# Kernel tuning notes

Measured on AMD Instinct MI355X. Metric: run time of the kernel, lower is better.

The kernel has to match this reference:

```python
import jax, jax.numpy as jnp
import numpy as np

B, LQ, LK, LS = 2, 2048, 2048, 256
HID, NH = 1024, 16
HD = HID // NH  # head_dim = 64


def setup_inputs() -> dict:
    key = jax.random.key(0)
    ks = jax.random.split(key, 14)
    s = 1.0 / np.sqrt(HID)
    inp = {
        "query": jax.random.normal(ks[0], (B, LQ, HID), jnp.float32),
        "sampled": jax.random.normal(ks[1], (B, LS, HID), jnp.float32),
        "key": jax.random.normal(ks[2], (B, LK, HID), jnp.float32),
        "value": jax.random.normal(ks[3], (B, LK, HID), jnp.float32),
        "Wq": jax.random.uniform(ks[4], (HID, HID), jnp.float32, -s, s),
        "bq": jax.random.uniform(ks[5], (HID,), jnp.float32, -s, s),
        "Wk": jax.random.uniform(ks[6], (HID, HID), jnp.float32, -s, s),
        "bk": jax.random.uniform(ks[7], (HID,), jnp.float32, -s, s),
        "Wv": jax.random.uniform(ks[8], (HID, HID), jnp.float32, -s, s),
        "bv": jax.random.uniform(ks[9], (HID,), jnp.float32, -s, s),
        "Wo": jax.random.uniform(ks[10], (HID, HID), jnp.float32, -s, s),
        "bo": jax.random.uniform(ks[11], (HID,), jnp.float32, -s, s),
        # fresh nn.Linear(LS+LK, LK) created each forward; fan_in = LS+LK
        "rW": jax.random.uniform(ks[12], (LK, LS + LK), jnp.float32, -1.0 / np.sqrt(LS + LK), 1.0 / np.sqrt(LS + LK)),
        "rb": jax.random.uniform(ks[13], (LK,), jnp.float32, -1.0 / np.sqrt(LS + LK), 1.0 / np.sqrt(LS + LK)),
    }
    return inp


def reference(query, sampled, key, value, Wq, bq, Wk, bk, Wv, bv, Wo, bo, rW, rb):
    scale = jnp.sqrt(jnp.float32(HD))
    Q = query @ Wq.T + bq                       # [B, LQ, HID]
    K = key @ Wk.T + bk                         # [B, LK, HID]
    V = value @ Wv.T + bv
    Kc = jnp.concatenate([sampled, K], axis=1)  # [B, LS+LK, HID]
    Vc = jnp.concatenate([sampled, V], axis=1)
    # seq-axis linear: out[b,t,h] = sum_s Kc[b,s,h] * rW[t,s] + rb[t]
    K = jnp.einsum("bsh,ts->bth", Kc, rW) + rb[None, :, None]  # [B, LK, HID]
    V = jnp.einsum("bsh,ts->bth", Vc, rW) + rb[None, :, None]
    # split heads: [B, NH, L, HD]
    Qh = Q.reshape(B, LQ, NH, HD).transpose(0, 2, 1, 3)
    Kh = K.reshape(B, LK, NH, HD).transpose(0, 2, 1, 3)
    Vh = V.reshape(B, LK, NH, HD).transpose(0, 2, 1, 3)
    energy = jnp.einsum("bhqd,bhkd->bhqk", Qh, Kh) / scale
    attention = jax.nn.softmax(energy, axis=-1)  # [B, NH, LQ, LK]
    x = jnp.einsum("bhqk,bhkd->bhqd", attention, Vh)
    x = x.transpose(0, 2, 1, 3).reshape(B, LQ, HID)
    x = x @ Wo.T + bo
    return x, attention
```

## Files before the change

### kernel.cpp

```cpp
#include <hip/hip_runtime.h>
#include <cstdint>
#include <cstddef>

#define NB   2
#define LQ   2048
#define LKK  2048
#define LS   256
#define HID  1024
#define NH   16
#define LSK  2304

#define DEV __device__ __forceinline__

typedef __bf16 bf16x8 __attribute__((ext_vector_type(8)));
typedef __bf16 bf16x4 __attribute__((ext_vector_type(4)));
typedef float  f32x4  __attribute__((ext_vector_type(4)));
typedef unsigned short us8 __attribute__((ext_vector_type(8)));

DEV unsigned short f2bf(float f) {
  unsigned int u = __builtin_bit_cast(unsigned int, f);
  u = (u + 0x7fffu + ((u >> 16) & 1u)) >> 16;
  return (unsigned short)u;
}
DEV bf16x8 ld_frag(const void* p) {
  uint4 v = *(const uint4*)p;
  return __builtin_bit_cast(bf16x8, v);
}
DEV void gload_lds16(const unsigned short* g, unsigned short* l) {
  __builtin_amdgcn_global_load_lds((const __attribute__((address_space(1))) unsigned int*)g,
                                   (__attribute__((address_space(3))) unsigned int*)l,
                                   16, 0, 0);
}
DEV float fexp2(float x) { float r; asm("v_exp_f32 %0, %1" : "=v"(r) : "v"(x)); return r; }

struct CastParams { const float* src[8]; unsigned short* dst[8]; int end8[8]; int total8; };

__global__ __launch_bounds__(256)
void cast_samp(CastParams p, const float* __restrict__ samp,
               unsigned short* __restrict__ KcT, unsigned short* __restrict__ VcT) {
  __shared__ unsigned short tl[64][65];
  const int tid = threadIdx.x;
  if (blockIdx.x < 128) {
    const int bid = blockIdx.x;
    const int st = bid & 3, nt = (bid >> 2) & 15, b = bid >> 6;
    const int nl = tid & 63, sq = tid >> 6;
#pragma unroll
    for (int j = 0; j < 16; ++j) {
      int sl = sq * 16 + j;
      tl[sl][nl] = f2bf(samp[(size_t)(b * LS + st * 64 + sl) * HID + nt * 64 + nl]);
    }
    __syncthreads();
#pragma unroll
    for (int wv = 0; wv < 2; ++wv) {
      int idx = wv * 256 + tid;
      int n_local = idx >> 3, sc = idx & 7;
      us8 v;
#pragma unroll
      for (int j = 0; j < 8; ++j) v[j] = tl[sc * 8 + j][n_local];
      size_t o = (size_t)(b * HID + nt * 64 + n_local) * LSK + st * 64 + sc * 8;
      *(us8*)(KcT + o) = v;
      *(us8*)(VcT + o) = v;
    }
    return;
  }
  const int stride = (gridDim.x - 128) * blockDim.x;
  for (int i = (blockIdx.x - 128) * blockDim.x + tid; i < p.total8; i += stride) {
    int s = 0;
    while (i >= p.end8[s]) ++s;
    int base = s ? p.end8[s - 1] : 0;
    size_t off = (size_t)(i - base) * 8;
    const float4* q = (const float4*)(p.src[s] + off);
    float4 a = q[0], b = q[1];
    us8 o;
    o[0] = f2bf(a.x); o[1] = f2bf(a.y); o[2] = f2bf(a.z); o[3] = f2bf(a.w);
    o[4] = f2bf(b.x); o[5] = f2bf(b.y); o[6] = f2bf(b.z); o[7] = f2bf(b.w);
    *(us8*)(p.dst[s] + off) = o;
  }
}

struct GDesc {
  const unsigned short* A;
  const unsigned short* BT;
  const float* bias;
  void* out0;
  void* out1;
  int ldo, moff, K, flags;
  float oscale;
};
struct GParams { GDesc d[6]; int per_z; int nt_n; int chunk; };

__global__ __launch_bounds__(256, 2)
void gemm_multi(GParams p) {
  __shared__ unsigned short lA[128 * 64];
  __shared__ unsigned short lB[128 * 64];
  const int bid = blockIdx.x;
  const int wid = (bid & 7) * p.chunk + (bid >> 3);
  const int z = wid / p.per_z;
  const int r = wid - z * p.per_z;
  const int n0 = (r % p.nt_n) * 128;
  const int m0 = (r / p.nt_n) * 128;
  const GDesc g = p.d[z];
  const int tid = threadIdx.x, l = tid & 63, w = tid >> 6;
  const int wr = w >> 1, wc = w & 1;
  const int K = g.K;
  const unsigned short* A = g.A;
  const unsigned short* BT = g.BT;
  f32x4 acc[4][4] = {};
  const int nk = K >> 6;
  for (int kt = 0; kt < nk; ++kt) {
    const int k0 = kt << 6;
#pragma unroll
    for (int it = 0; it < 4; ++it) {
      int s = it * 256 + tid;
      int t = s >> 3, c = s & 7, g2 = c ^ (t & 7);
      gload_lds16(A + (size_t)(m0 + t) * K + (k0 + g2 * 8), lA + (size_t)s * 8);
      gload_lds16(BT + (size_t)(n0 + t) * K + (k0 + g2 * 8), lB + (size_t)s * 8);
    }
    __syncthreads();
#pragma unroll
    for (int ks = 0; ks < 2; ++ks) {
      bf16x8 af[4], bfr[4];
#pragma unroll
      for (int mi = 0; mi < 4; ++mi) {
        int row = wr * 64 + mi * 16 + (l & 15);
        int ch = (ks * 4 + (l >> 4)) ^ (row & 7);
        af[mi] = ld_frag((const char*)lA + row * 128 + ch * 16);
      }
#pragma unroll
      for (int ni = 0; ni < 4; ++ni) {
        int row = wc * 64 + ni * 16 + (l & 15);
        int ch = (ks * 4 + (l >> 4)) ^ (row & 7);
        bfr[ni] = ld_frag((const char*)lB + row * 128 + ch * 16);
      }
#pragma unroll
      for (int mi = 0; mi < 4; ++mi)
#pragma unroll
        for (int ni = 0; ni < 4; ++ni)
          acc[mi][ni] = __builtin_amdgcn_mfma_f32_16x16x32_bf16(af[mi], bfr[ni], acc[mi][ni], 0, 0, 0);
    }
    __syncthreads();
  }
  const int epi = g.flags & 15, brow = (g.flags >> 4) & 1;
  const int r4 = (l >> 4) * 4;
#pragma unroll
  for (int mi = 0; mi < 4; ++mi) {
    const int mbase = m0 + wr * 64 + mi * 16 + r4;
#pragma unroll
    for (int ni = 0; ni < 4; ++ni) {
      const int n = n0 + wc * 64 + ni * 16 + (l & 15);
      f32x4 v = acc[mi][ni];
      if (brow) {
#pragma unroll
        for (int rr = 0; rr < 4; ++rr) v[rr] = (v[rr] + g.bias[mbase + rr]) * g.oscale;
      } else {
        const float bn = g.bias[n];
#pragma unroll
        for (int rr = 0; rr < 4; ++rr) v[rr] = (v[rr] + bn) * g.oscale;
      }
      if (epi == 0) {
        unsigned short* o = (unsigned short*)g.out0;
#pragma unroll
        for (int rr = 0; rr < 4; ++rr) o[(size_t)(mbase + rr) * g.ldo + n] = f2bf(v[rr]);
      } else if (epi == 1) {
        unsigned short* o = (unsigned short*)g.out0;
        ushort4 pk;
        pk.x = f2bf(v[0]); pk.y = f2bf(v[1]); pk.z = f2bf(v[2]); pk.w = f2bf(v[3]);
        *(ushort4*)(o + (size_t)n * g.ldo + g.moff + mbase) = pk;
      } else if (epi == 2) {
        float* o = (float*)g.out0;
#pragma unroll
        for (int rr = 0; rr < 4; ++rr) o[(size_t)(mbase + rr) * g.ldo + n] = v[rr];
      } else {
        if (n < 2048) {
          unsigned short* o = (unsigned short*)g.out0 + (size_t)(n >> 10) * LQ * HID;
#pragma unroll
          for (int rr = 0; rr < 4; ++rr) o[(size_t)(mbase + rr) * HID + (n & 1023)] = f2bf(v[rr]);
        } else {
          unsigned short* o = (unsigned short*)g.out1 + (size_t)((n >> 10) - 2) * HID * LKK;
          ushort4 pk;
          pk.x = f2bf(v[0]); pk.y = f2bf(v[1]); pk.z = f2bf(v[2]); pk.w = f2bf(v[3]);
          *(ushort4*)(o + (size_t)(n & 1023) * LKK + mbase) = pk;
        }
      }
    }
  }
}

__global__ __launch_bounds__(256, 2)
void attn_fused(const unsigned short* __restrict__ Qb, const unsigned short* __restrict__ Kn,
                const unsigned short* __restrict__ Vt, float* __restrict__ attn_out,
                unsigned short* __restrict__ xpre) {
  __shared__ unsigned short smem[24576];
  const int tid = threadIdx.x, l = tid & 63, w = tid >> 6;
  const int bid = blockIdx.x;
  const int wid = (bid & 7) * 64 + (bid >> 3);
  const int qt = wid & 15, bh = wid >> 4, b = bh >> 4, h = bh & 15;
  const unsigned short* Qg = Qb + (size_t)(b * LQ + qt * 128) * HID + h * 64;
  const unsigned short* Kg = Kn + (size_t)(b * LKK) * HID + h * 64;
  const unsigned short* Vg = Vt + ((size_t)b * HID + h * 64) * LKK;
  unsigned short* const lK0 = smem;
  unsigned short* const lK1 = smem + 4096;
  unsigned short* const lV0 = smem + 8192;
  unsigned short* const lV1 = smem + 12288;
  unsigned short* const bufA = smem;
  unsigned short* const bufB = smem + 8192;
  unsigned short* const lPw = smem + 16384 + w * 2048;

#pragma unroll
  for (int it = 0; it < 4; ++it) {
    int s = it * 256 + tid, t = s >> 3, c = s & 7, g2 = c ^ (t & 7);
    gload_lds16(Qg + (size_t)t * HID + g2 * 8, smem + (size_t)s * 8);
  }
  __syncthreads();
  bf16x8 qf[2][2];
#pragma unroll
  for (int qi = 0; qi < 2; ++qi)
#pragma unroll
    for (int ds = 0; ds < 2; ++ds) {
      int row = w * 32 + qi * 16 + (l & 15);
      int ch = (ds * 4 + (l >> 4)) ^ (row & 7);
      qf[qi][ds] = ld_frag((const char*)smem + row * 128 + ch * 16);
    }
  __syncthreads();

  auto stageK128 = [&](int kt, unsigned short* dst) {
#pragma unroll
    for (int it = 0; it < 4; ++it) {
      int s = it * 256 + tid, t = s >> 3, c = s & 7, g2 = c ^ (t & 7);
      gload_lds16(Kg + (size_t)(kt * 128 + t) * HID + g2 * 8, dst + (size_t)s * 8);
    }
  };
  auto stageK = [&](int kt, unsigned short* dst) {
#pragma unroll
    for (int it = 0; it < 2; ++it) {
      int s = it * 256 + tid, t = s >> 3, c = s & 7, g2 = c ^ (t & 7);
      gload_lds16(Kg + (size_t)(kt * 64 + t) * HID + g2 * 8, dst + (size_t)s * 8);
    }
  };
  auto stageV = [&](int kt, unsigned short* dst) {
#pragma unroll
    for (int it = 0; it < 2; ++it) {
      int s = it * 256 + tid, t = s >> 3, c = s & 7, g2 = c ^ (t & 7);
      gload_lds16(Vg + (size_t)t * LKK + kt * 64 + g2 * 8, dst + (size_t)s * 8);
    }
  };

  float sm[2] = { 0.0f, 0.0f };
  stageK128(0, bufA);
  __syncthreads();
  for (int kt = 0; kt < 16; ++kt) {
    if (kt < 15) stageK128(kt + 1, (kt & 1) ? bufA : bufB);
    const unsigned short* cK = (kt & 1) ? bufB : bufA;
#pragma unroll
    for (int half = 0; half < 2; ++half) {
      f32x4 e[4][2] = {};
      __builtin_amdgcn_s_setprio(1);
#pragma unroll
      for (int ds = 0; ds < 2; ++ds) {
        bf16x8 kf[4];
#pragma unroll
        for (int ki = 0; ki < 4; ++ki) {
          int row = half * 64 + ki * 16 + (l & 15);
          int ch = (ds * 4 + (l >> 4)) ^ (row & 7);
          kf[ki] = ld_frag((const char*)cK + row * 128 + ch * 16);
        }
#pragma unroll
        for (int ki = 0; ki < 4; ++ki)
#pragma unroll
          for (int qi = 0; qi < 2; ++qi)
            e[ki][qi] = __builtin_amdgcn_mfma_f32_16x16x32_bf16(kf[ki], qf[qi][ds], e[ki][qi], 0, 0, 0);
      }
      __builtin_amdgcn_s_setprio(0);
#pragma unroll
      for (int qi = 0; qi < 2; ++qi) {
        float s0 = 0.f, s1 = 0.f, s2 = 0.f, s3 = 0.f;
#pragma unroll
        for (int ki = 0; ki < 4; ++ki) {
          s0 += fexp2(e[ki][qi][0]);
          s1 += fexp2(e[ki][qi][1]);
          s2 += fexp2(e[ki][qi][2]);
          s3 += fexp2(e[ki][qi][3]);
        }
        sm[qi] += (s0 + s1) + (s2 + s3);
      }
    }
    __syncthreads();
  }
  float rinv[2];
#pragma unroll
  for (int qi = 0; qi < 2; ++qi) {
    float ss = sm[qi];
    ss += __shfl_xor(ss, 16, 64);
    ss += __shfl_xor(ss, 32, 64);
    rinv[qi] = 1.0f / ss;
  }

  stageK(0, lK0); stageV(0, lV0);
  asm volatile("s_waitcnt vmcnt(0)" ::: "memory");
  __builtin_amdgcn_sched_barrier(0);
  __builtin_amdgcn_s_barrier();
  __builtin_amdgcn_sched_barrier(0);
  f32x4 x[2][4] = {};
  float* attn_base = attn_out + ((size_t)bh * LQ + qt * 128 + w * 32) * LKK;
  for (int kt = 0; kt < 32; ++kt) {
    if (kt < 31) {
      stageK(kt + 1, (kt & 1) ? lK0 : lK1);
      stageV(kt + 1, (kt & 1) ? lV0 : lV1);
    }
    __builtin_amdgcn_sched_barrier(0);
    const unsigned short* cK = (kt & 1) ? lK1 : lK0;
    const unsigned short* cV = (kt & 1) ? lV1 : lV0;
    f32x4 e[4][2] = {};
    __builtin_amdgcn_s_setprio(1);
#pragma unroll
    for (int ds = 0; ds < 2; ++ds) {
      bf16x8 kf[4];
#pragma unroll
      for (int ki = 0; ki < 4; ++ki) {
        int row = ki * 16 + (l & 15);
        int ch = (ds * 4 + (l >> 4)) ^ (row & 7);
        kf[ki] = ld_frag((const char*)cK + row * 128 + ch * 16);
      }
#pragma unroll
      for (int ki = 0; ki < 4; ++ki)
#pragma unroll
        for (int qi = 0; qi < 2; ++qi)
          e[ki][qi] = __builtin_amdgcn_mfma_f32_16x16x32_bf16(kf[ki], qf[qi][ds], e[ki][qi], 0, 0, 0);
    }
    __builtin_amdgcn_s_setprio(0);
#pragma unroll
    for (int qi = 0; qi < 2; ++qi) {
      const int q = qi * 16 + (l & 15);
      float* arow = attn_base + (size_t)q * LKK + kt * 64 + ((l >> 4) << 2);
#pragma unroll
      for (int ki = 0; ki < 4; ++ki) {
        float p0 = fexp2(e[ki][qi][0]) * rinv[qi];
        float p1 = fexp2(e[ki][qi][1]) * rinv[qi];
        float p2 = fexp2(e[ki][qi][2]) * rinv[qi];
        float p3 = fexp2(e[ki][qi][3]) * rinv[qi];
        float4 st; st.x = p0; st.y = p1; st.z = p2; st.w = p3;
        *(float4*)(arow + ki * 16) = st;
        bf16x4 pk;
        pk[0] = (__bf16)p0; pk[1] = (__bf16)p1; pk[2] = (__bf16)p2; pk[3] = (__bf16)p3;
        int chv = (ki * 2 + (l >> 5)) ^ (q & 7);
        *(bf16x4*)(lPw + q * 64 + chv * 8 + ((l >> 4) & 1) * 4) = pk;
      }
    }
    asm volatile("s_waitcnt lgkmcnt(0)" ::: "memory");
    __builtin_amdgcn_sched_barrier(0);
    __builtin_amdgcn_s_setprio(1);
#pragma unroll
    for (int ks = 0; ks < 2; ++ks) {
      bf16x8 pa[2], vb[4];
#pragma unroll
      for (int qi = 0; qi < 2; ++qi) {
        int row = qi * 16 + (l & 15);
        int ch = (ks * 4 + (l >> 4)) ^ (row & 7);
        pa[qi] = ld_frag((const char*)lPw + row * 128 + ch * 16);
      }
#pragma unroll
      for (int df = 0; df < 4; ++df) {
        int row = df * 16 + (l & 15);
        int ch = (ks * 4 + (l >> 4)) ^ (row & 7);
        vb[df] = ld_frag((const char*)cV + row * 128 + ch * 16);
      }
#pragma unroll
      for (int qi = 0; qi < 2; ++qi)
#pragma unroll
        for (int df = 0; df < 4; ++df)
          x[qi][df] = __builtin_amdgcn_mfma_f32_16x16x32_bf16(pa[qi], vb[df], x[qi][df], 0, 0, 0);
    }
    __builtin_amdgcn_s_setprio(0);
    asm volatile("s_waitcnt vmcnt(8)" ::: "memory");
    __builtin_amdgcn_sched_barrier(0);
    __builtin_amdgcn_s_barrier();
    __builtin_amdgcn_sched_barrier(0);
  }
#pragma unroll
  for (int qi = 0; qi < 2; ++qi)
#pragma unroll
    for (int df = 0; df < 4; ++df)
#pragma unroll
      for (int r = 0; r < 4; ++r)
        xpre[(size_t)(b * LQ + qt * 128 + w * 32 + qi * 16 + (l >> 4) * 4 + r) * HID
             + h * 64 + df * 16 + (l & 15)] = f2bf(x[qi][df][r]);
}

extern "C" void kernel_launch(void* const* d_in, const int* in_sizes, int n_in,
                              void* d_out, int out_size, void* d_ws, size_t ws_size,
                              hipStream_t stream) {
  (void)in_sizes; (void)n_in; (void)out_size; (void)ws_size;
  const float* query   = (const float*)d_in[0];
  const float* sampled = (const float*)d_in[1];
  const float* key     = (const float*)d_in[2];
  const float* value   = (const float*)d_in[3];
  const float* Wq = (const float*)d_in[4];  const float* bq = (const float*)d_in[5];
  const float* Wk = (const float*)d_in[6];  const float* bk = (const float*)d_in[7];
  const float* Wv = (const float*)d_in[8];  const float* bv = (const float*)d_in[9];
  const float* Wo = (const float*)d_in[10]; const float* bo = (const float*)d_in[11];
  const float* rW = (const float*)d_in[12]; const float* rb = (const float*)d_in[13];

  char* ws = (char*)d_ws;
  unsigned short* qb   = (unsigned short*)(ws + 0);
  unsigned short* keyb = (unsigned short*)(ws + 8388608);
  unsigned short* valb = (unsigned short*)(ws + 16777216);
  unsigned short* Wqb  = (unsigned short*)(ws + 25165824);
  unsigned short* Wkb  = (unsigned short*)(ws + 27262976);
  unsigned short* Wvb  = (unsigned short*)(ws + 29360128);
  unsigned short* Wob  = (unsigned short*)(ws + 31457280);
  unsigned short* rWb  = (unsigned short*)(ws + 33554432);
  unsigned short* Qbf  = (unsigned short*)(ws + 42991616);
  unsigned short* KcT  = (unsigned short*)(ws + 51380224);
  unsigned short* VcT  = (unsigned short*)(ws + 60817408);
  unsigned short* Knew = (unsigned short*)(ws + 70254592);
  unsigned short* Vt   = (unsigned short*)(ws + 78643200);
  unsigned short* xpre = (unsigned short*)(ws + 87031808);

  float* out_x    = (float*)d_out;
  float* out_attn = out_x + (size_t)NB * LQ * HID;

  CastParams cp{};
  const float* srcs[8] = { query, key, value, Wq, Wk, Wv, Wo, rW };
  unsigned short* dsts[8] = { qb, keyb, valb, Wqb, Wkb, Wvb, Wob, rWb };
  const int sz8[8] = { 524288, 524288, 524288, 131072, 131072, 131072, 131072, 589824 };
  int acc = 0;
  for (int i = 0; i < 8; ++i) { cp.src[i] = srcs[i]; cp.dst[i] = dsts[i]; acc += sz8[i]; cp.end8[i] = acc; }
  cp.total8 = acc;
  cast_samp<<<2176, 256, 0, stream>>>(cp, sampled, KcT, VcT);

  GParams pp{};
  for (int b = 0; b < 2; ++b) {
    pp.d[b]     = { qb   + (size_t)b * 2048 * 1024, Wqb, bq,
                    (void*)(Qbf + (size_t)b * 2048 * 1024), nullptr, 1024, 0, 1024, 0, 0.180336880f };
    pp.d[2 + b] = { keyb + (size_t)b * 2048 * 1024, Wkb, bk,
                    (void*)(KcT + (size_t)b * HID * LSK), nullptr, LSK, LS, 1024, 1, 1.0f };
    pp.d[4 + b] = { valb + (size_t)b * 2048 * 1024, Wvb, bv,
                    (void*)(VcT + (size_t)b * HID * LSK), nullptr, LSK, LS, 1024, 1, 1.0f };
  }
  pp.per_z = 128; pp.nt_n = 8; pp.chunk = 96;
  gemm_multi<<<768, 256, 0, stream>>>(pp);

  GParams sp{};
  sp.d[0] = { rWb, KcT, rb, (void*)Knew, (void*)Vt, 0, 0, LSK, 4 | 16, 1.0f };
  sp.per_z = 512; sp.nt_n = 32; sp.chunk = 64;
  gemm_multi<<<512, 256, 0, stream>>>(sp);

  attn_fused<<<512, 256, 0, stream>>>(Qbf, Knew, Vt, out_attn, xpre);

  GParams op{};
  op.d[0] = { xpre, Wob, bo, (void*)out_x, nullptr, 1024, 0, 1024, 2, 1.0f };
  op.per_z = 256; op.nt_n = 8; op.chunk = 32;
  gemm_multi<<<256, 256, 0, stream>>>(op);
}
```

Before: 325.8 us.

## Coalesce attention-probability stores via LDS and triple-buffer K/V staging

Attention probabilities are no longer written straight from MFMA registers as scattered float4 stores. Each wave re-reads its bf16 P tile from LDS and writes contiguous 256-byte row segments with nontemporal stores. K/V staging moves from double to triple buffering with a prefetch distance of two tiles, and the vmcnt waits and LDS footprint are adjusted to match. The stored attention values are now bf16-rounded before being widened back to fp32, which lowers output precision. More LDS per block may also limit occupancy.

Result: faster. 270.9 us (-16.8%).

```diff
diff --git a/kernel.cpp b/kernel.cpp
--- a/kernel.cpp
+++ b/kernel.cpp
@@ -21,6 +21,10 @@
   unsigned int u = __builtin_bit_cast(unsigned int, f);
   u = (u + 0x7fffu + ((u >> 16) & 1u)) >> 16;
   return (unsigned short)u;
+}
+DEV float bf2f(unsigned short h) {
+  unsigned int u = ((unsigned int)h) << 16;
+  return __builtin_bit_cast(float, u);
 }
 DEV bf16x8 ld_frag(const void* p) {
   uint4 v = *(const uint4*)p;
@@ -190,7 +194,7 @@
 void attn_fused(const unsigned short* __restrict__ Qb, const unsigned short* __restrict__ Kn,
                 const unsigned short* __restrict__ Vt, float* __restrict__ attn_out,
                 unsigned short* __restrict__ xpre) {
-  __shared__ unsigned short smem[24576];
+  __shared__ unsigned short smem[32768];
   const int tid = threadIdx.x, l = tid & 63, w = tid >> 6;
   const int bid = blockIdx.x;
   const int wid = (bid & 7) * 64 + (bid >> 3);
@@ -198,13 +202,9 @@
   const unsigned short* Qg = Qb + (size_t)(b * LQ + qt * 128) * HID + h * 64;
   const unsigned short* Kg = Kn + (size_t)(b * LKK) * HID + h * 64;
   const unsigned short* Vg = Vt + ((size_t)b * HID + h * 64) * LKK;
-  unsigned short* const lK0 = smem;
-  unsigned short* const lK1 = smem + 4096;
-  unsigned short* const lV0 = smem + 8192;
-  unsigned short* const lV1 = smem + 12288;
   unsigned short* const bufA = smem;
   unsigned short* const bufB = smem + 8192;
-  unsigned short* const lPw = smem + 16384 + w * 2048;
+  unsigned short* const lPw = smem + 24576 + w * 2048;
 
 #pragma unroll
   for (int it = 0; it < 4; ++it) {
@@ -295,21 +295,24 @@
     rinv[qi] = 1.0f / ss;
   }
 
-  stageK(0, lK0); stageV(0, lV0);
-  asm volatile("s_waitcnt vmcnt(0)" ::: "memory");
+  stageK(0, smem); stageV(0, smem + 12288);
+  stageK(1, smem + 4096); stageV(1, smem + 16384);
+  asm volatile("s_waitcnt vmcnt(4)" ::: "memory");
   __builtin_amdgcn_sched_barrier(0);
   __builtin_amdgcn_s_barrier();
   __builtin_amdgcn_sched_barrier(0);
   f32x4 x[2][4] = {};
   float* attn_base = attn_out + ((size_t)bh * LQ + qt * 128 + w * 32) * LKK;
   for (int kt = 0; kt < 32; ++kt) {
-    if (kt < 31) {
-      stageK(kt + 1, (kt & 1) ? lK0 : lK1);
-      stageV(kt + 1, (kt & 1) ? lV0 : lV1);
+    if (kt < 30) {
+      int slot = (kt + 2) % 3;
+      stageK(kt + 2, smem + slot * 4096);
+      stageV(kt + 2, smem + 12288 + slot * 4096);
     }
     __builtin_amdgcn_sched_barrier(0);
-    const unsigned short* cK = (kt & 1) ? lK1 : lK0;
-    const unsigned short* cV = (kt & 1) ? lV1 : lV0;
+    const int cs = kt % 3;
+    const unsigned short* cK = smem + cs * 4096;
+    const unsigned short* cV = smem + 12288 + cs * 4096;
     f32x4 e[4][2] = {};
     __builtin_amdgcn_s_setprio(1);
 #pragma unroll
@@ -331,15 +334,12 @@
 #pragma unroll
     for (int qi = 0; qi < 2; ++qi) {
       const int q = qi * 16 + (l & 15);
-      float* arow = attn_base + (size_t)q * LKK + kt * 64 + ((l >> 4) << 2);
 #pragma unroll
       for (int ki = 0; ki < 4; ++ki) {
         float p0 = fexp2(e[ki][qi][0]) * rinv[qi];
         float p1 = fexp2(e[ki][qi][1]) * rinv[qi];
         float p2 = fexp2(e[ki][qi][2]) * rinv[qi];
         float p3 = fexp2(e[ki][qi][3]) * rinv[qi];
-        float4 st; st.x = p0; st.y = p1; st.z = p2; st.w = p3;
-        *(float4*)(arow + ki * 16) = st;
         bf16x4 pk;
         pk[0] = (__bf16)p0; pk[1] = (__bf16)p1; pk[2] = (__bf16)p2; pk[3] = (__bf16)p3;
         int chv = (ki * 2 + (l >> 5)) ^ (q & 7);
@@ -348,6 +348,19 @@
     }
     asm volatile("s_waitcnt lgkmcnt(0)" ::: "memory");
     __builtin_amdgcn_sched_barrier(0);
+    {
+      float* abase = attn_base + kt * 64;
+#pragma unroll
+      for (int ps = 0; ps < 8; ++ps) {
+        int rq = ps * 4 + (l >> 4);
+        int c16 = l & 15;
+        const unsigned short* src = lPw + rq * 64 + (((c16 >> 1) ^ (rq & 7)) << 3) + (c16 & 1) * 4;
+        ushort4 hv = *(const ushort4*)src;
+        f32x4 f;
+        f[0] = bf2f(hv.x); f[1] = bf2f(hv.y); f[2] = bf2f(hv.z); f[3] = bf2f(hv.w);
+        __builtin_nontemporal_store(f, (f32x4*)(abase + (size_t)rq * LKK + c16 * 4));
+      }
+    }
     __builtin_amdgcn_s_setprio(1);
 #pragma unroll
     for (int ks = 0; ks < 2; ++ks) {
@@ -371,10 +384,14 @@
           x[qi][df] = __builtin_amdgcn_mfma_f32_16x16x32_bf16(pa[qi], vb[df], x[qi][df], 0, 0, 0);
     }
     __builtin_amdgcn_s_setprio(0);
-    asm volatile("s_waitcnt vmcnt(8)" ::: "memory");
-    __builtin_amdgcn_sched_barrier(0);
-    __builtin_amdgcn_s_barrier();
-    __builtin_amdgcn_sched_barrier(0);
+    if (kt < 31) {
+      if (kt == 0)       { asm volatile("s_waitcnt vmcnt(12)" ::: "memory"); }
+      else if (kt < 30)  { asm volatile("s_waitcnt vmcnt(20)" ::: "memory"); }
+      else               { asm volatile("s_waitcnt vmcnt(16)" ::: "memory"); }
+      __builtin_amdgcn_sched_barrier(0);
+      __builtin_amdgcn_s_barrier();
+      __builtin_amdgcn_sched_barrier(0);
+    }
   }
 #pragma unroll
   for (int qi = 0; qi < 2; ++qi)
```
